# Performance work log

Hardware: AMD Instinct MI355X
Metric: run time of the kernel (lower is better)

Reference implementation:

```python
import jax, jax.numpy as jnp
import numpy as np

B, N, D, H = 256, 256, 136, 128  # queries, docs/query, feature dim, hidden dim


def setup_inputs() -> dict:
    key = jax.random.key(0)
    ks = jax.random.split(key, 7)
    features = jax.random.uniform(ks[0], (B, N, D), dtype=jnp.float32)
    labels = jax.random.randint(ks[1], (B, N), 0, 5, dtype=jnp.int32)  # relevance grades 0..4
    # Small init scales keep MLP scores in (-1, 1) so log2(1 + max(s_i, s_j)) is well-defined
    W1 = jax.random.normal(ks[2], (D, H), dtype=jnp.float32) * 0.05
    b1 = jnp.zeros((H,), dtype=jnp.float32)
    W2 = jax.random.normal(ks[3], (H, H), dtype=jnp.float32) * 0.05
    b2 = jnp.zeros((H,), dtype=jnp.float32)
    W3 = jax.random.normal(ks[4], (H, 1), dtype=jnp.float32) * 0.02
    b3 = jnp.zeros((1,), dtype=jnp.float32)
    return {"features": features, "labels": labels,
            "W1": W1, "b1": b1, "W2": W2, "b2": b2, "W3": W3, "b3": b3}


def _scores(features, W1, b1, W2, b2, W3, b3):
    # Linear-ReLU-(Dropout: identity in eval)-Linear-ReLU-Linear, then squeeze(-1)
    h = jax.nn.relu(jnp.einsum('bnd,dh->bnh', features, W1) + b1)
    h = jax.nn.relu(jnp.einsum('bnh,hk->bnk', h, W2) + b2)
    return (jnp.einsum('bnh,ho->bno', h, W3) + b3).squeeze(-1)  # [B, N]


def _compute_lambdas(scores, labels):
    si = scores[:, :, None]        # s_i  [B, N, 1]
    sj = scores[:, None, :]        # s_j  [B, 1, N]
    li = labels[:, :, None]
    lj = labels[:, None, :]
    # lambda_ij = 0.5 * (1 - sigmoid(s_j - s_i)) = 0.5 * sigmoid(s_i - s_j)
    lam = 0.5 * jax.nn.sigmoid(si - sj)
    gain = jnp.exp2(labels.astype(scores.dtype))  # 2 ** l
    dndcg = jnp.abs((gain[:, :, None] - gain[:, None, :])
                    / (1.0 + jnp.log2(1.0 + jnp.maximum(si, sj))))
    A = jnp.where(li > lj, lam * dndcg, jnp.zeros((), scores.dtype))  # [B, N, N]
    # lambdas[i] += A[i, j] over j (pairs where l_i > l_j); lambdas[j] -= A[i, j]
    return A.sum(-1) - A.sum(-2)  # [B, N]


def reference(features, labels, W1, b1, W2, b2, W3, b3):
    scores = _scores(features, W1, b1, W2, b2, W3, b3)
    return _compute_lambdas(scores, labels)
```

## Files before the change

### kernel.cpp

```cpp
#include <hip/hip_runtime.h>
#include <hip/hip_bf16.h>

#define DIN  136
#define HH   128
#define NSEQ 256
#define NB   256
#define BROWS 128
#define SKS  136

typedef __attribute__((ext_vector_type(4))) float f32x4;
typedef __attribute__((ext_vector_type(2))) float f32x2;
typedef __attribute__((ext_vector_type(8))) short bf16x8;

static __device__ __forceinline__ unsigned short f2bf(float f) {
    unsigned int u = __float_as_uint(f);
    u += 0x7fffu + ((u >> 16) & 1u);
    return (unsigned short)(u >> 16);
}

__global__ __launch_bounds__(256)
void scores_mfma_kernel(const float* __restrict__ features,
                        const int*   __restrict__ labels,
                        const float* __restrict__ W1, const float* __restrict__ b1,
                        const float* __restrict__ W2, const float* __restrict__ b2,
                        const float* __restrict__ W3, const float* __restrict__ b3,
                        float4* __restrict__ pack,
                        float* __restrict__ out_zero)
{
    __shared__ short a_lds[BROWS * SKS];
    __shared__ short w_lds[HH * SKS];

    const int t    = threadIdx.x;
    const int lane = t & 63;
    const int wv   = t >> 6;
    const int l15  = lane & 15;
    const int l4   = lane >> 4;
    const long row0 = (long)blockIdx.x * BROWS;

    {
        const f32x2* src = (const f32x2*)(features + row0 * DIN);
        for (int i = t; i < BROWS * DIN / 2; i += 256) {
            f32x2 v = src[i];
            unsigned int p = (unsigned int)f2bf(v.x) | ((unsigned int)f2bf(v.y) << 16);
            ((unsigned int*)a_lds)[i] = p;
        }
    }
    {
        const f32x2* src = (const f32x2*)W1;
        for (int i = t; i < DIN * HH / 2; i += 256) {
            f32x2 v = src[i];
            const int e = i * 2, k = e >> 7, n = e & 127;
            w_lds[n * SKS + k]       = (short)f2bf(v.x);
            w_lds[(n + 1) * SKS + k] = (short)f2bf(v.y);
        }
    }
    __syncthreads();

    f32x4 acc[2][8];
#pragma unroll
    for (int tn = 0; tn < 8; ++tn) {
        const float bv = b1[tn * 16 + l15];
#pragma unroll
        for (int tm = 0; tm < 2; ++tm) acc[tm][tn] = (f32x4){bv, bv, bv, bv};
    }
    for (int kc = 0; kc < 5; ++kc) {
        bf16x8 afr[2], bfr[8];
        if (kc < 4) {
            const int kb = kc * 32 + l4 * 8;
#pragma unroll
            for (int tm = 0; tm < 2; ++tm)
                afr[tm] = *(const bf16x8*)&a_lds[((wv * 2 + tm) * 16 + l15) * SKS + kb];
#pragma unroll
            for (int tn = 0; tn < 8; ++tn)
                bfr[tn] = *(const bf16x8*)&w_lds[(tn * 16 + l15) * SKS + kb];
        } else {
            if (l4 == 0) {
#pragma unroll
                for (int tm = 0; tm < 2; ++tm)
                    afr[tm] = *(const bf16x8*)&a_lds[((wv * 2 + tm) * 16 + l15) * SKS + 128];
#pragma unroll
                for (int tn = 0; tn < 8; ++tn)
                    bfr[tn] = *(const bf16x8*)&w_lds[(tn * 16 + l15) * SKS + 128];
            } else {
#pragma unroll
                for (int tm = 0; tm < 2; ++tm) afr[tm] = (bf16x8){0,0,0,0,0,0,0,0};
#pragma unroll
                for (int tn = 0; tn < 8; ++tn) bfr[tn] = (bf16x8){0,0,0,0,0,0,0,0};
            }
        }
#pragma unroll
        for (int tm = 0; tm < 2; ++tm)
#pragma unroll
            for (int tn = 0; tn < 8; ++tn)
                acc[tm][tn] = __builtin_amdgcn_mfma_f32_16x16x32_bf16(
                    afr[tm], bfr[tn], acc[tm][tn], 0, 0, 0);
    }
    __syncthreads();

#pragma unroll
    for (int tm = 0; tm < 2; ++tm) {
        const int rbase = (wv * 2 + tm) * 16 + l4 * 4;
#pragma unroll
        for (int tn = 0; tn < 8; ++tn) {
            const int col = tn * 16 + l15;
#pragma unroll
            for (int j = 0; j < 4; ++j)
                a_lds[(rbase + j) * SKS + col] = (short)f2bf(fmaxf(acc[tm][tn][j], 0.f));
        }
    }
    {
        const f32x2* src = (const f32x2*)W2;
        for (int i = t; i < HH * HH / 2; i += 256) {
            f32x2 v = src[i];
            const int e = i * 2, k = e >> 7, n = e & 127;
            w_lds[n * SKS + k]       = (short)f2bf(v.x);
            w_lds[(n + 1) * SKS + k] = (short)f2bf(v.y);
        }
    }
    __syncthreads();

    f32x4 acc2[2][8];
#pragma unroll
    for (int tn = 0; tn < 8; ++tn) {
        const float bv = b2[tn * 16 + l15];
#pragma unroll
        for (int tm = 0; tm < 2; ++tm) acc2[tm][tn] = (f32x4){bv, bv, bv, bv};
    }
    for (int kc = 0; kc < 4; ++kc) {
        const int kb = kc * 32 + l4 * 8;
        bf16x8 afr[2], bfr[8];
#pragma unroll
        for (int tm = 0; tm < 2; ++tm)
            afr[tm] = *(const bf16x8*)&a_lds[((wv * 2 + tm) * 16 + l15) * SKS + kb];
#pragma unroll
        for (int tn = 0; tn < 8; ++tn)
            bfr[tn] = *(const bf16x8*)&w_lds[(tn * 16 + l15) * SKS + kb];
#pragma unroll
        for (int tm = 0; tm < 2; ++tm)
#pragma unroll
            for (int tn = 0; tn < 8; ++tn)
                acc2[tm][tn] = __builtin_amdgcn_mfma_f32_16x16x32_bf16(
                    afr[tm], bfr[tn], acc2[tm][tn], 0, 0, 0);
    }

    {
        float w3v[8];
#pragma unroll
        for (int tn = 0; tn < 8; ++tn) w3v[tn] = W3[tn * 16 + l15];
        const float b3v = b3[0];
#pragma unroll
        for (int tm = 0; tm < 2; ++tm) {
#pragma unroll
            for (int j = 0; j < 4; ++j) {
                float p = 0.f;
#pragma unroll
                for (int tn = 0; tn < 8; ++tn)
                    p += fmaxf(acc2[tm][tn][j], 0.f) * w3v[tn];
                p += __shfl_xor(p, 1, 64);
                p += __shfl_xor(p, 2, 64);
                p += __shfl_xor(p, 4, 64);
                p += __shfl_xor(p, 8, 64);
                if (l15 == 0) {
                    const int row = (wv * 2 + tm) * 16 + l4 * 4 + j;
                    const long gr = row0 + row;
                    const float s = p + b3v;
                    const int lab = labels[gr];
                    const float g = exp2f((float)lab);
                    const float disc = 1.f / (1.f + log2f(1.f + s));
                    pack[gr] = make_float4(s, g, disc, __int_as_float(lab));
                    out_zero[gr] = 0.f;
                }
            }
        }
    }
}

__global__ __launch_bounds__(256)
void lambda_pair_kernel(const float4* __restrict__ pack,
                        float* __restrict__ out)
{
    __shared__ float4 sp[NSEQ];
    const int t  = threadIdx.x;
    const int b  = blockIdx.x >> 2;
    const int jq = blockIdx.x & 3;

    const float4 me = pack[b * NSEQ + t];
    sp[t] = me;
    __syncthreads();

    const float si = me.x, gi = me.y, di = me.z;
    const int   li = __float_as_int(me.w);

    float accum = 0.f;
    const int j0 = jq * 64;
#pragma unroll 8
    for (int jj = 0; jj < 64; ++jj) {
        const float4 o = sp[j0 + jj];
        const float sj = o.x, gj = o.y, dj = o.z;
        const int   lj = __float_as_int(o.w);
        const float dmax = (si > sj) ? di : dj;
        const float dn   = fabsf(gi - gj) * dmax;
        const float e    = exp2f((sj - si) * 1.44269504f);
        const float sig  = __builtin_amdgcn_rcpf(1.f + e);
        const float w    = (li > lj) ? sig : (sig - 1.f);
        accum += 0.5f * dn * w;
    }
    atomicAdd(&out[b * NSEQ + t], accum);
}

extern "C" void kernel_launch(void* const* d_in, const int* in_sizes, int n_in,
                              void* d_out, int out_size, void* d_ws, size_t ws_size,
                              hipStream_t stream)
{
    const float* features = (const float*)d_in[0];
    const int*   labels   = (const int*)d_in[1];
    const float* W1 = (const float*)d_in[2];
    const float* b1 = (const float*)d_in[3];
    const float* W2 = (const float*)d_in[4];
    const float* b2 = (const float*)d_in[5];
    const float* W3 = (const float*)d_in[6];
    const float* b3 = (const float*)d_in[7];

    float4* pack = (float4*)d_ws;
    float*  out  = (float*)d_out;

    scores_mfma_kernel<<<NB * NSEQ / BROWS, 256, 0, stream>>>(
        features, labels, W1, b1, W2, b2, W3, b3, pack, out);
    lambda_pair_kernel<<<NB * 4, 256, 0, stream>>>(pack, out);
}
```

Measured before the change: 126.8 us.

## Pre-transpose weights to bf16 once, halve scores tile, simplify pair loop

A new prep kernel converts W1 and W2 to transposed, padded bf16 buffers in workspace once per call. The scores kernel then reads weight fragments directly from global/L2 instead of staging them in LDS. The row tile drops from 128 to 64, which doubles the block count and shrinks LDS use. The pair kernel now splits the j range 8 ways instead of 4, and it folds the log2e and 0.5 factors into the packed values. It also replaces the label comparison with the sign of the gain difference, which drops the label field. The costs are an extra kernel launch, uncached-in-LDS weight reads repeated across blocks, and more atomics.

```diff
diff --git a/kernel.cpp b/kernel.cpp
--- a/kernel.cpp
+++ b/kernel.cpp
@@ -5,8 +5,9 @@
 #define HH   128
 #define NSEQ 256
 #define NB   256
-#define BROWS 128
-#define SKS  136
+#define BROWS 64
+#define K1P  168
+#define JB   8
 
 typedef __attribute__((ext_vector_type(4))) float f32x4;
 typedef __attribute__((ext_vector_type(2))) float f32x2;
@@ -19,16 +20,32 @@
 }
 
 __global__ __launch_bounds__(256)
+void prep_kernel(const float* __restrict__ W1, const float* __restrict__ W2,
+                 short* __restrict__ w1t, short* __restrict__ w2t)
+{
+    const int nt = gridDim.x * 256;
+    const int idx = blockIdx.x * 256 + threadIdx.x;
+    for (int e = idx; e < HH * K1P; e += nt) {
+        const int n = e / K1P, k = e - n * K1P;
+        w1t[e] = (k < DIN) ? (short)f2bf(W1[k * HH + n]) : (short)0;
+    }
+    for (int e = idx; e < HH * HH; e += nt) {
+        const int n = e >> 7, k = e & 127;
+        w2t[e] = (short)f2bf(W2[k * HH + n]);
+    }
+}
+
+__global__ __launch_bounds__(256)
 void scores_mfma_kernel(const float* __restrict__ features,
                         const int*   __restrict__ labels,
-                        const float* __restrict__ W1, const float* __restrict__ b1,
-                        const float* __restrict__ W2, const float* __restrict__ b2,
+                        const short* __restrict__ w1t,
+                        const short* __restrict__ w2t,
+                        const float* __restrict__ b1, const float* __restrict__ b2,
                         const float* __restrict__ W3, const float* __restrict__ b3,
                         float4* __restrict__ pack,
                         float* __restrict__ out_zero)
 {
-    __shared__ short a_lds[BROWS * SKS];
-    __shared__ short w_lds[HH * SKS];
+    __shared__ short a_lds[BROWS * K1P];
 
     const int t    = threadIdx.x;
     const int lane = t & 63;
@@ -41,106 +58,65 @@
         const f32x2* src = (const f32x2*)(features + row0 * DIN);
         for (int i = t; i < BROWS * DIN / 2; i += 256) {
             f32x2 v = src[i];
-            unsigned int p = (unsigned int)f2bf(v.x) | ((unsigned int)f2bf(v.y) << 16);
-            ((unsigned int*)a_lds)[i] = p;
+            const int e = i * 2;
+            const int r = e / DIN, k = e - r * DIN;
+            *(unsigned int*)&a_lds[r * K1P + k] =
+                (unsigned int)f2bf(v.x) | ((unsigned int)f2bf(v.y) << 16);
         }
-    }
-    {
-        const f32x2* src = (const f32x2*)W1;
-        for (int i = t; i < DIN * HH / 2; i += 256) {
-            f32x2 v = src[i];
-            const int e = i * 2, k = e >> 7, n = e & 127;
-            w_lds[n * SKS + k]       = (short)f2bf(v.x);
-            w_lds[(n + 1) * SKS + k] = (short)f2bf(v.y);
+        for (int i = t; i < BROWS * 16; i += 256) {
+            const int r = i >> 4, k = DIN + (i & 15) * 2;
+            *(unsigned int*)&a_lds[r * K1P + k] = 0u;
         }
     }
     __syncthreads();
 
-    f32x4 acc[2][8];
+    const int arow = (wv * 16 + l15) * K1P;
+
+    f32x4 acc[8];
 #pragma unroll
     for (int tn = 0; tn < 8; ++tn) {
         const float bv = b1[tn * 16 + l15];
-#pragma unroll
-        for (int tm = 0; tm < 2; ++tm) acc[tm][tn] = (f32x4){bv, bv, bv, bv};
+        acc[tn] = (f32x4){bv, bv, bv, bv};
     }
     for (int kc = 0; kc < 5; ++kc) {
-        bf16x8 afr[2], bfr[8];
-        if (kc < 4) {
-            const int kb = kc * 32 + l4 * 8;
-#pragma unroll
-            for (int tm = 0; tm < 2; ++tm)
-                afr[tm] = *(const bf16x8*)&a_lds[((wv * 2 + tm) * 16 + l15) * SKS + kb];
-#pragma unroll
-            for (int tn = 0; tn < 8; ++tn)
-                bfr[tn] = *(const bf16x8*)&w_lds[(tn * 16 + l15) * SKS + kb];
-        } else {
-            if (l4 == 0) {
-#pragma unroll
-                for (int tm = 0; tm < 2; ++tm)
-                    afr[tm] = *(const bf16x8*)&a_lds[((wv * 2 + tm) * 16 + l15) * SKS + 128];
-#pragma unroll
-                for (int tn = 0; tn < 8; ++tn)
-                    bfr[tn] = *(const bf16x8*)&w_lds[(tn * 16 + l15) * SKS + 128];
-            } else {
-#pragma unroll
-                for (int tm = 0; tm < 2; ++tm) afr[tm] = (bf16x8){0,0,0,0,0,0,0,0};
-#pragma unroll
-                for (int tn = 0; tn < 8; ++tn) bfr[tn] = (bf16x8){0,0,0,0,0,0,0,0};
-            }
-        }
-#pragma unroll
-        for (int tm = 0; tm < 2; ++tm)
-#pragma unroll
-            for (int tn = 0; tn < 8; ++tn)
-                acc[tm][tn] = __builtin_amdgcn_mfma_f32_16x16x32_bf16(
-                    afr[tm], bfr[tn], acc[tm][tn], 0, 0, 0);
-    }
-    __syncthreads();
-
-#pragma unroll
-    for (int tm = 0; tm < 2; ++tm) {
-        const int rbase = (wv * 2 + tm) * 16 + l4 * 4;
-#pragma unroll
-        for (int tn = 0; tn < 8; ++tn) {
-            const int col = tn * 16 + l15;
-#pragma unroll
-            for (int j = 0; j < 4; ++j)
-                a_lds[(rbase + j) * SKS + col] = (short)f2bf(fmaxf(acc[tm][tn][j], 0.f));
-        }
-    }
-    {
-        const f32x2* src = (const f32x2*)W2;
-        for (int i = t; i < HH * HH / 2; i += 256) {
-            f32x2 v = src[i];
-            const int e = i * 2, k = e >> 7, n = e & 127;
-            w_lds[n * SKS + k]       = (short)f2bf(v.x);
-            w_lds[(n + 1) * SKS + k] = (short)f2bf(v.y);
-        }
-    }
-    __syncthreads();
-
-    f32x4 acc2[2][8];
+        const int kb = kc * 32 + l4 * 8;
+        const bf16x8 afr = *(const bf16x8*)&a_lds[arow + kb];
+        bf16x8 bfr[8];
+#pragma unroll
+        for (int tn = 0; tn < 8; ++tn)
+            bfr[tn] = *(const bf16x8*)&w1t[(tn * 16 + l15) * K1P + kb];
+#pragma unroll
+        for (int tn = 0; tn < 8; ++tn)
+            acc[tn] = __builtin_amdgcn_mfma_f32_16x16x32_bf16(afr, bfr[tn], acc[tn], 0, 0, 0);
+    }
+    __syncthreads();
+
+#pragma unroll
+    for (int tn = 0; tn < 8; ++tn) {
+        const int col = tn * 16 + l15;
+#pragma unroll
+        for (int j = 0; j < 4; ++j)
+            a_lds[(wv * 16 + l4 * 4 + j) * K1P + col] =
+                (short)f2bf(fmaxf(acc[tn][j], 0.f));
+    }
+    __syncthreads();
+
+    f32x4 acc2[8];
 #pragma unroll
     for (int tn = 0; tn < 8; ++tn) {
         const float bv = b2[tn * 16 + l15];
-#pragma unroll
-        for (int tm = 0; tm < 2; ++tm) acc2[tm][tn] = (f32x4){bv, bv, bv, bv};
+        acc2[tn] = (f32x4){bv, bv, bv, bv};
     }
     for (int kc = 0; kc < 4; ++kc) {
         const int kb = kc * 32 + l4 * 8;
-        bf16x8 afr[2], bfr[8];
-#pragma unroll
-        for (int tm = 0; tm < 2; ++tm)
-            afr[tm] = *(const bf16x8*)&a_lds[((wv * 2 + tm) * 16 + l15) * SKS + kb];
-#pragma unroll
-        for (int tn = 0; tn < 8; ++tn)
-            bfr[tn] = *(const bf16x8*)&w_lds[(tn * 16 + l15) * SKS + kb];
-#pragma unroll
-        for (int tm = 0; tm < 2; ++tm)
-#pragma unroll
-            for (int tn = 0; tn < 8; ++tn)
-                acc2[tm][tn] = __builtin_amdgcn_mfma_f32_16x16x32_bf16(
-                    afr[tm], bfr[tn], acc2[tm][tn], 0, 0, 0);
+        const bf16x8 afr = *(const bf16x8*)&a_lds[arow + kb];
+        bf16x8 bfr[8];
+#pragma unroll
+        for (int tn = 0; tn < 8; ++tn)
+            bfr[tn] = *(const bf16x8*)&w2t[(tn * 16 + l15) * HH + kb];
+#pragma unroll
+        for (int tn = 0; tn < 8; ++tn)
+            acc2[tn] = __builtin_amdgcn_mfma_f32_16x16x32_bf16(afr, bfr[tn], acc2[tn], 0, 0, 0);
     }
 
     {
@@ -149,27 +125,25 @@
         for (int tn = 0; tn < 8; ++tn) w3v[tn] = W3[tn * 16 + l15];
         const float b3v = b3[0];
 #pragma unroll
-        for (int tm = 0; tm < 2; ++tm) {
-#pragma unroll
-            for (int j = 0; j < 4; ++j) {
-                float p = 0.f;
-#pragma unroll
-                for (int tn = 0; tn < 8; ++tn)
-                    p += fmaxf(acc2[tm][tn][j], 0.f) * w3v[tn];
-                p += __shfl_xor(p, 1, 64);
-                p += __shfl_xor(p, 2, 64);
-                p += __shfl_xor(p, 4, 64);
-                p += __shfl_xor(p, 8, 64);
-                if (l15 == 0) {
-                    const int row = (wv * 2 + tm) * 16 + l4 * 4 + j;
-                    const long gr = row0 + row;
-                    const float s = p + b3v;
-                    const int lab = labels[gr];
-                    const float g = exp2f((float)lab);
-                    const float disc = 1.f / (1.f + log2f(1.f + s));
-                    pack[gr] = make_float4(s, g, disc, __int_as_float(lab));
-                    out_zero[gr] = 0.f;
-                }
+        for (int j = 0; j < 4; ++j) {
+            float p = 0.f;
+#pragma unroll
+            for (int tn = 0; tn < 8; ++tn)
+                p += fmaxf(acc2[tn][j], 0.f) * w3v[tn];
+            p += __shfl_xor(p, 1, 64);
+            p += __shfl_xor(p, 2, 64);
+            p += __shfl_xor(p, 4, 64);
+            p += __shfl_xor(p, 8, 64);
+            if (l15 == 0) {
+                const int row = wv * 16 + l4 * 4 + j;
+                const long gr = row0 + row;
+                const float s = p + b3v;
+                const int lab = labels[gr];
+                const float g = 0.5f * exp2f((float)lab);
+                const float disc = 1.f / (1.f + log2f(1.f + s));
+                pack[gr] = make_float4(s * 1.44269504088896f,
+                                       g, disc, 0.f);
+                out_zero[gr] = 0.f;
             }
         }
     }
@@ -181,29 +155,25 @@
 {
     __shared__ float4 sp[NSEQ];
     const int t  = threadIdx.x;
-    const int b  = blockIdx.x >> 2;
-    const int jq = blockIdx.x & 3;
+    const int b  = blockIdx.x >> 3;
+    const int jo = (blockIdx.x & 7) * (NSEQ / JB);
 
     const float4 me = pack[b * NSEQ + t];
     sp[t] = me;
     __syncthreads();
 
-    const float si = me.x, gi = me.y, di = me.z;
-    const int   li = __float_as_int(me.w);
-
+    const float sci = me.x, gi = me.y, di = me.z;
     float accum = 0.f;
-    const int j0 = jq * 64;
 #pragma unroll 8
-    for (int jj = 0; jj < 64; ++jj) {
-        const float4 o = sp[j0 + jj];
-        const float sj = o.x, gj = o.y, dj = o.z;
-        const int   lj = __float_as_int(o.w);
-        const float dmax = (si > sj) ? di : dj;
-        const float dn   = fabsf(gi - gj) * dmax;
-        const float e    = exp2f((sj - si) * 1.44269504f);
-        const float sig  = __builtin_amdgcn_rcpf(1.f + e);
-        const float w    = (li > lj) ? sig : (sig - 1.f);
-        accum += 0.5f * dn * w;
+    for (int jj = 0; jj < NSEQ / JB; ++jj) {
+        const float4 o = sp[jo + jj];
+        const float dg = o.y - gi;
+        const float e  = exp2f(o.x - sci);
+        const float r  = __builtin_amdgcn_rcpf(1.f + e);
+        const float dmax = (sci > o.x) ? di : o.z;
+        const float dn = fabsf(dg) * dmax;
+        const float w  = (dg < 0.f) ? r : (r - 1.f);
+        accum += dn * w;
     }
     atomicAdd(&out[b * NSEQ + t], accum);
 }
@@ -222,9 +192,12 @@
     const float* b3 = (const float*)d_in[7];
 
     float4* pack = (float4*)d_ws;
+    short*  w1t  = (short*)((char*)d_ws + (size_t)NB * NSEQ * 16);
+    short*  w2t  = w1t + HH * K1P;
     float*  out  = (float*)d_out;
 
+    prep_kernel<<<64, 256, 0, stream>>>(W1, W2, w1t, w2t);
     scores_mfma_kernel<<<NB * NSEQ / BROWS, 256, 0, stream>>>(
-        features, labels, W1, b1, W2, b2, W3, b3, pack, out);
-    lambda_pair_kernel<<<NB * 4, 256, 0, stream>>>(pack, out);
-}
+        features, labels, w1t, w2t, b1, b2, W3, b3, pack, out);
+    lambda_pair_kernel<<<NB * JB, 256, 0, stream>>>(pack, out);
+}
```

New measurement: 124.4 us. About the same (-1.9%).
